# Kernel optimization log

Hardware: AMD Instinct MI355X
Metric: run time of the kernel (lower is better)

## Reference

```python
import jax, jax.numpy as jnp
import numpy as np

B, S, D = 128, 1024, 1024  # batch, seq_len, dim (ctx_dim == dim)


def setup_inputs() -> dict:
    key = jax.random.key(0)
    k1, k2, k3, k4, k5 = jax.random.split(key, 5)
    h = jax.random.normal(k1, (B, D), dtype=jnp.float32)
    context = jax.random.normal(k2, (B, S, D), dtype=jnp.float32)
    mask = jax.random.randint(k3, (B, S), 0, 2).astype(bool)
    # scale weights like nn.Linear default init (~U(-1/sqrt(fan_in), 1/sqrt(fan_in)))
    W_in = jax.random.normal(k4, (D, D), dtype=jnp.float32) / np.sqrt(D)
    W_out = jax.random.normal(k5, (D, 2 * D), dtype=jnp.float32) / np.sqrt(2 * D)
    return {"h": h, "context": context, "mask": mask, "W_in": W_in, "W_out": W_out}


def reference(h, context, mask, W_in, W_out):
    # target = linear_in(h): [B, ctx_dim]
    target = h @ W_in.T
    # attention scores: bmm(context, target) -> [B, S]
    attn = jnp.einsum('bsd,bd->bs', context, target)
    attn = jnp.where(mask, -jnp.inf, attn)
    attn = jax.nn.softmax(attn, axis=1)
    # weighted context: [B, D]
    weighted_context = jnp.einsum('bs,bsd->bd', attn, context)
    h_tilde = jnp.tanh(jnp.concatenate([weighted_context, h], axis=1) @ W_out.T)
    return (h_tilde, attn)
```

## Files before the change

kernel.cpp:

```cpp
#include <hip/hip_runtime.h>
#include <hip/hip_bf16.h>
#include <math.h>

#define BB 128
#define SS 1024
#define DD 1024
#define NC 8
#define SC (SS / NC)

#define OFF_TARGET 0
#define OFF_SCORES (BB * DD)
#define OFF_M      (OFF_SCORES + BB * SS)
#define OFF_L      (OFF_M + BB * NC)
#define OFF_WCP    (OFF_L + BB * NC)
#define OFF_WC     (OFF_WCP + BB * NC * DD)
#define OFF_FLAG   (OFF_WC + BB * DD)

__global__ void detect_mask(const unsigned char* __restrict__ mask,
                            int* __restrict__ flag)
{
    if (threadIdx.x == 0) {
        int isInt32 = 1;
        for (int i = 0; i < 256; ++i) {
            unsigned char b0 = mask[4 * i + 0];
            unsigned char b1 = mask[4 * i + 1];
            unsigned char b2 = mask[4 * i + 2];
            unsigned char b3 = mask[4 * i + 3];
            if (b1 | b2 | b3) { isInt32 = 0; break; }
            if (b0 > 1)       { isInt32 = 0; break; }
        }
        *flag = isInt32;
    }
}

__global__ __launch_bounds__(256) void gemm_nt(
    const float* __restrict__ A0, const float* __restrict__ A1,
    const float* __restrict__ Bm, float* __restrict__ Cout,
    int M, int N, int K, int applyTanh)
{
    __shared__ float As[16][64];
    __shared__ float Bs[32][65];

    const int tid  = threadIdx.x;
    const int bn0  = blockIdx.x * 32;
    const int bm0  = blockIdx.y * 16;
    const int r    = tid >> 5;
    const int ccol = tid & 31;

    const int ar = tid >> 4;
    const int ak = (tid & 15) << 2;

    float acc0 = 0.f, acc1 = 0.f;

    for (int k0 = 0; k0 < K; k0 += 64) {
        const float* Asrc = A0;
        int kk = k0;
        if (A1 != nullptr && k0 >= 1024) { Asrc = A1; kk = k0 - 1024; }
        float4 av = *(const float4*)(Asrc + (size_t)(bm0 + ar) * 1024 + kk + ak);
        *(float4*)&As[ar][ak] = av;

        #pragma unroll
        for (int u = 0; u < 2; ++u) {
            int idx4 = tid + u * 256;
            int c    = idx4 >> 4;
            int k    = (idx4 & 15) << 2;
            float4 bv = *(const float4*)(Bm + (size_t)(bn0 + c) * K + k0 + k);
            Bs[c][k + 0] = bv.x;
            Bs[c][k + 1] = bv.y;
            Bs[c][k + 2] = bv.z;
            Bs[c][k + 3] = bv.w;
        }
        __syncthreads();

        #pragma unroll
        for (int k = 0; k < 64; ++k) {
            float bv = Bs[ccol][k];
            acc0 = fmaf(As[r][k],     bv, acc0);
            acc1 = fmaf(As[r + 8][k], bv, acc1);
        }
        __syncthreads();
    }

    const int col = bn0 + ccol;
    float v0 = applyTanh ? tanhf(acc0) : acc0;
    float v1 = applyTanh ? tanhf(acc1) : acc1;
    Cout[(size_t)(bm0 + r) * N + col]     = v0;
    Cout[(size_t)(bm0 + r + 8) * N + col] = v1;
}

__global__ __launch_bounds__(256) void attn_pass(
    const float* __restrict__ ctx, const float* __restrict__ tgt,
    const unsigned char* __restrict__ mask_u8,
    const int* __restrict__ mask_flag,
    float* __restrict__ scores, float* __restrict__ m_part,
    float* __restrict__ l_part, float* __restrict__ wc_part)
{
    const int b    = blockIdx.y;
    const int ch   = blockIdx.x;
    const int tid  = threadIdx.x;
    const int w    = tid >> 6;
    const int lane = tid & 63;
    const int s0   = ch * SC;

    const int mflag = *mask_flag;
    const int* mask_i32 = (const int*)mask_u8;

    float4 t4[4];
    const float4* tp = (const float4*)(tgt + (size_t)b * DD);
    #pragma unroll
    for (int j = 0; j < 4; ++j) t4[j] = tp[j * 64 + lane];

    float m = -INFINITY, l = 0.f;
    float4 acc[4];
    #pragma unroll
    for (int j = 0; j < 4; ++j) acc[j] = make_float4(0.f, 0.f, 0.f, 0.f);

    float* srow = scores + (size_t)b * SS;

    for (int i = 0; i < SC / 4; ++i) {
        const int s = s0 + w + i * 4;
        const float4* row = (const float4*)(ctx + ((size_t)b * SS + s) * DD);
        float4 c4[4];
        #pragma unroll
        for (int j = 0; j < 4; ++j) c4[j] = row[j * 64 + lane];

        float part = 0.f;
        #pragma unroll
        for (int j = 0; j < 4; ++j) {
            part = fmaf(c4[j].x, t4[j].x, part);
            part = fmaf(c4[j].y, t4[j].y, part);
            part = fmaf(c4[j].z, t4[j].z, part);
            part = fmaf(c4[j].w, t4[j].w, part);
        }
        #pragma unroll
        for (int off = 32; off >= 1; off >>= 1)
            part += __shfl_xor(part, off, 64);

        const int mraw = mflag ? mask_i32[(size_t)b * SS + s]
                               : (int)mask_u8[(size_t)b * SS + s];
        const bool mk = (mraw != 0);
        const float sc = mk ? -INFINITY : part;
        if (lane == 0) srow[s] = sc;

        if (sc > m) {
            const float f = __expf(m - sc);
            l *= f;
            #pragma unroll
            for (int j = 0; j < 4; ++j) {
                acc[j].x *= f; acc[j].y *= f; acc[j].z *= f; acc[j].w *= f;
            }
            m = sc;
        }
        const float p = mk ? 0.f : __expf(sc - m);
        l += p;
        #pragma unroll
        for (int j = 0; j < 4; ++j) {
            acc[j].x = fmaf(p, c4[j].x, acc[j].x);
            acc[j].y = fmaf(p, c4[j].y, acc[j].y);
            acc[j].z = fmaf(p, c4[j].z, acc[j].z);
            acc[j].w = fmaf(p, c4[j].w, acc[j].w);
        }
    }

    __shared__ float sm[4], sl[4];
    __shared__ float sacc[4][DD];
    if (lane == 0) { sm[w] = m; sl[w] = l; }
    #pragma unroll
    for (int j = 0; j < 4; ++j)
        *(float4*)&sacc[w][j * 256 + lane * 4] = acc[j];
    __syncthreads();

    const float mb = fmaxf(fmaxf(sm[0], sm[1]), fmaxf(sm[2], sm[3]));
    const float f0 = __expf(sm[0] - mb);
    const float f1 = __expf(sm[1] - mb);
    const float f2 = __expf(sm[2] - mb);
    const float f3 = __expf(sm[3] - mb);
    const float lb = sl[0] * f0 + sl[1] * f1 + sl[2] * f2 + sl[3] * f3;

    const int d0 = tid * 4;
    float4 a0 = *(float4*)&sacc[0][d0];
    float4 a1 = *(float4*)&sacc[1][d0];
    float4 a2 = *(float4*)&sacc[2][d0];
    float4 a3 = *(float4*)&sacc[3][d0];
    float4 o;
    o.x = a0.x * f0 + a1.x * f1 + a2.x * f2 + a3.x * f3;
    o.y = a0.y * f0 + a1.y * f1 + a2.y * f2 + a3.y * f3;
    o.z = a0.z * f0 + a1.z * f1 + a2.z * f2 + a3.z * f3;
    o.w = a0.w * f0 + a1.w * f1 + a2.w * f2 + a3.w * f3;
    *(float4*)(wc_part + ((size_t)b * NC + ch) * DD + d0) = o;

    if (tid == 0) {
        m_part[b * NC + ch] = mb;
        l_part[b * NC + ch] = lb;
    }
}

__global__ __launch_bounds__(256) void combine(
    const float* __restrict__ m_part, const float* __restrict__ l_part,
    const float* __restrict__ wc_part, const float* __restrict__ scores,
    float* __restrict__ wc, float* __restrict__ attn_out)
{
    const int b = blockIdx.x;
    const int tid = threadIdx.x;

    float M = -INFINITY;
    #pragma unroll
    for (int c = 0; c < NC; ++c) M = fmaxf(M, m_part[b * NC + c]);
    float fc[NC];
    float L = 0.f;
    #pragma unroll
    for (int c = 0; c < NC; ++c) {
        fc[c] = __expf(m_part[b * NC + c] - M);
        L = fmaf(l_part[b * NC + c], fc[c], L);
    }
    const float invL = 1.f / L;

    const int d0 = tid * 4;
    float4 v = make_float4(0.f, 0.f, 0.f, 0.f);
    #pragma unroll
    for (int c = 0; c < NC; ++c) {
        float4 pv = *(const float4*)(wc_part + ((size_t)b * NC + c) * DD + d0);
        v.x = fmaf(pv.x, fc[c], v.x);
        v.y = fmaf(pv.y, fc[c], v.y);
        v.z = fmaf(pv.z, fc[c], v.z);
        v.w = fmaf(pv.w, fc[c], v.w);
    }
    v.x *= invL; v.y *= invL; v.z *= invL; v.w *= invL;
    *(float4*)(wc + (size_t)b * DD + d0) = v;

    for (int s = tid; s < SS; s += 256)
        attn_out[(size_t)b * SS + s] = __expf(scores[(size_t)b * SS + s] - M) * invL;
}

extern "C" void kernel_launch(void* const* d_in, const int* in_sizes, int n_in,
                              void* d_out, int out_size, void* d_ws, size_t ws_size,
                              hipStream_t stream)
{
    (void)in_sizes; (void)n_in; (void)out_size; (void)ws_size;

    const float* h     = (const float*)d_in[0];
    const float* ctx   = (const float*)d_in[1];
    const unsigned char* mask = (const unsigned char*)d_in[2];
    const float* W_in  = (const float*)d_in[3];
    const float* W_out = (const float*)d_in[4];

    float* out_h    = (float*)d_out;
    float* out_attn = out_h + (size_t)BB * DD;

    float* ws      = (float*)d_ws;
    float* target  = ws + OFF_TARGET;
    float* scores  = ws + OFF_SCORES;
    float* m_part  = ws + OFF_M;
    float* l_part  = ws + OFF_L;
    float* wc_part = ws + OFF_WCP;
    float* wc      = ws + OFF_WC;
    int*   mflag   = (int*)(ws + OFF_FLAG);

    detect_mask<<<1, 64, 0, stream>>>(mask, mflag);

    gemm_nt<<<dim3(32, 8), 256, 0, stream>>>(h, nullptr, W_in, target,
                                             BB, DD, 1024, 0);

    attn_pass<<<dim3(NC, BB), 256, 0, stream>>>(ctx, target, mask, mflag,
                                                scores, m_part, l_part, wc_part);

    combine<<<dim3(BB), 256, 0, stream>>>(m_part, l_part, wc_part, scores,
                                          wc, out_attn);

    gemm_nt<<<dim3(32, 8), 256, 0, stream>>>(wc, h, W_out, out_h,
                                             BB, DD, 2048, 1);
}
```

Before: 817.2 us.

## Use split-K register-tiled GEMMs and process four context rows per attention step

Replaces the small 16x32 GEMM with a 64x64 register-blocked tile (4x4 outputs per thread) split over K into eight partial buffers. A separate reduction kernel sums the partials and applies tanh. The attention pass now loads four contiguous rows per wave per step, so it batches the shuffle reductions, mask loads and online-softmax rescaling. The mask-detection loop is also parallelised across the wave. The cost is extra workspace traffic for the partials, two more kernel launches, and more registers per thread in the attention kernel.

```diff
diff --git a/kernel.cpp b/kernel.cpp
--- a/kernel.cpp
+++ b/kernel.cpp
@@ -7,85 +7,124 @@
 #define DD 1024
 #define NC 8
 #define SC (SS / NC)
-
-#define OFF_TARGET 0
-#define OFF_SCORES (BB * DD)
-#define OFF_M      (OFF_SCORES + BB * SS)
-#define OFF_L      (OFF_M + BB * NC)
-#define OFF_WCP    (OFF_L + BB * NC)
-#define OFF_WC     (OFF_WCP + BB * NC * DD)
-#define OFF_FLAG   (OFF_WC + BB * DD)
+#define KSPLIT 8
+
+#define OFF_TGT_PART 0
+#define OFF_TARGET   (OFF_TGT_PART + KSPLIT * BB * DD)
+#define OFF_SCORES   (OFF_TARGET + BB * DD)
+#define OFF_M        (OFF_SCORES + BB * SS)
+#define OFF_L        (OFF_M + BB * NC)
+#define OFF_WCP      (OFF_L + BB * NC)
+#define OFF_WC       (OFF_WCP + BB * NC * DD)
+#define OFF_OUT_PART (OFF_WC + BB * DD)
+#define OFF_FLAG     (OFF_OUT_PART + KSPLIT * BB * DD)
 
 __global__ void detect_mask(const unsigned char* __restrict__ mask,
                             int* __restrict__ flag)
 {
-    if (threadIdx.x == 0) {
-        int isInt32 = 1;
-        for (int i = 0; i < 256; ++i) {
-            unsigned char b0 = mask[4 * i + 0];
-            unsigned char b1 = mask[4 * i + 1];
-            unsigned char b2 = mask[4 * i + 2];
-            unsigned char b3 = mask[4 * i + 3];
-            if (b1 | b2 | b3) { isInt32 = 0; break; }
-            if (b0 > 1)       { isInt32 = 0; break; }
-        }
-        *flag = isInt32;
-    }
-}
-
-__global__ __launch_bounds__(256) void gemm_nt(
+    const int tid = threadIdx.x;
+    int ok = 1;
+    for (int i = tid; i < 256; i += 64) {
+        unsigned char b0 = mask[4 * i + 0];
+        unsigned char b1 = mask[4 * i + 1];
+        unsigned char b2 = mask[4 * i + 2];
+        unsigned char b3 = mask[4 * i + 3];
+        if ((b1 | b2 | b3) != 0 || b0 > 1) ok = 0;
+    }
+    int all_ok = __all(ok);
+    if (tid == 0) *flag = all_ok;
+}
+
+__global__ __launch_bounds__(256) void gemm_splitk(
     const float* __restrict__ A0, const float* __restrict__ A1,
-    const float* __restrict__ Bm, float* __restrict__ Cout,
-    int M, int N, int K, int applyTanh)
-{
-    __shared__ float As[16][64];
-    __shared__ float Bs[32][65];
-
-    const int tid  = threadIdx.x;
-    const int bn0  = blockIdx.x * 32;
-    const int bm0  = blockIdx.y * 16;
-    const int r    = tid >> 5;
-    const int ccol = tid & 31;
-
-    const int ar = tid >> 4;
-    const int ak = (tid & 15) << 2;
-
-    float acc0 = 0.f, acc1 = 0.f;
-
-    for (int k0 = 0; k0 < K; k0 += 64) {
+    const float* __restrict__ W, float* __restrict__ Cpart,
+    int N, int K)
+{
+    __shared__ float As_t[64][64];
+    __shared__ float Bs_t[64][64];
+
+    const int tid = threadIdx.x;
+    const int bn0 = blockIdx.x * 64;
+    const int bm0 = blockIdx.y * 64;
+    const int kchunk = K / KSPLIT;
+    const int kbase = blockIdx.z * kchunk;
+
+    const int lrow = tid >> 2;
+    const int lk   = (tid & 3) * 16;
+    const int tr4  = (tid >> 4) * 4;
+    const int tc4  = (tid & 15) * 4;
+
+    float4 acc[4];
+    #pragma unroll
+    for (int r = 0; r < 4; ++r) acc[r] = make_float4(0.f, 0.f, 0.f, 0.f);
+
+    for (int k0 = kbase; k0 < kbase + kchunk; k0 += 64) {
         const float* Asrc = A0;
         int kk = k0;
         if (A1 != nullptr && k0 >= 1024) { Asrc = A1; kk = k0 - 1024; }
-        float4 av = *(const float4*)(Asrc + (size_t)(bm0 + ar) * 1024 + kk + ak);
-        *(float4*)&As[ar][ak] = av;
-
-        #pragma unroll
-        for (int u = 0; u < 2; ++u) {
-            int idx4 = tid + u * 256;
-            int c    = idx4 >> 4;
-            int k    = (idx4 & 15) << 2;
-            float4 bv = *(const float4*)(Bm + (size_t)(bn0 + c) * K + k0 + k);
-            Bs[c][k + 0] = bv.x;
-            Bs[c][k + 1] = bv.y;
-            Bs[c][k + 2] = bv.z;
-            Bs[c][k + 3] = bv.w;
+
+        #pragma unroll
+        for (int j = 0; j < 4; ++j) {
+            float4 av = *(const float4*)(Asrc + (size_t)(bm0 + lrow) * 1024 + kk + lk + 4 * j);
+            As_t[lk + 4 * j + 0][lrow] = av.x;
+            As_t[lk + 4 * j + 1][lrow] = av.y;
+            As_t[lk + 4 * j + 2][lrow] = av.z;
+            As_t[lk + 4 * j + 3][lrow] = av.w;
+            float4 wv = *(const float4*)(W + (size_t)(bn0 + lrow) * K + k0 + lk + 4 * j);
+            Bs_t[lk + 4 * j + 0][lrow] = wv.x;
+            Bs_t[lk + 4 * j + 1][lrow] = wv.y;
+            Bs_t[lk + 4 * j + 2][lrow] = wv.z;
+            Bs_t[lk + 4 * j + 3][lrow] = wv.w;
         }
         __syncthreads();
 
         #pragma unroll
         for (int k = 0; k < 64; ++k) {
-            float bv = Bs[ccol][k];
-            acc0 = fmaf(As[r][k],     bv, acc0);
-            acc1 = fmaf(As[r + 8][k], bv, acc1);
+            float4 a = *(const float4*)&As_t[k][tr4];
+            float4 b = *(const float4*)&Bs_t[k][tc4];
+            acc[0].x = fmaf(a.x, b.x, acc[0].x);
+            acc[0].y = fmaf(a.x, b.y, acc[0].y);
+            acc[0].z = fmaf(a.x, b.z, acc[0].z);
+            acc[0].w = fmaf(a.x, b.w, acc[0].w);
+            acc[1].x = fmaf(a.y, b.x, acc[1].x);
+            acc[1].y = fmaf(a.y, b.y, acc[1].y);
+            acc[1].z = fmaf(a.y, b.z, acc[1].z);
+            acc[1].w = fmaf(a.y, b.w, acc[1].w);
+            acc[2].x = fmaf(a.z, b.x, acc[2].x);
+            acc[2].y = fmaf(a.z, b.y, acc[2].y);
+            acc[2].z = fmaf(a.z, b.z, acc[2].z);
+            acc[2].w = fmaf(a.z, b.w, acc[2].w);
+            acc[3].x = fmaf(a.w, b.x, acc[3].x);
+            acc[3].y = fmaf(a.w, b.y, acc[3].y);
+            acc[3].z = fmaf(a.w, b.z, acc[3].z);
+            acc[3].w = fmaf(a.w, b.w, acc[3].w);
         }
         __syncthreads();
     }
 
-    const int col = bn0 + ccol;
-    float v0 = applyTanh ? tanhf(acc0) : acc0;
-    float v1 = applyTanh ? tanhf(acc1) : acc1;
-    Cout[(size_t)(bm0 + r) * N + col]     = v0;
-    Cout[(size_t)(bm0 + r + 8) * N + col] = v1;
+    float* base = Cpart + ((size_t)blockIdx.z * BB + bm0 + tr4) * N + bn0 + tc4;
+    #pragma unroll
+    for (int r = 0; r < 4; ++r)
+        *(float4*)(base + (size_t)r * N) = acc[r];
+}
+
+__global__ __launch_bounds__(256) void reduce_part(
+    const float* __restrict__ part, float* __restrict__ out,
+    int n4, int applyTanh)
+{
+    const int i = blockIdx.x * 256 + threadIdx.x;
+    if (i >= n4) return;
+    const float4* p4 = (const float4*)part;
+    float4 s = p4[i];
+    #pragma unroll
+    for (int ks = 1; ks < KSPLIT; ++ks) {
+        float4 v = p4[(size_t)ks * n4 + i];
+        s.x += v.x; s.y += v.y; s.z += v.z; s.w += v.w;
+    }
+    if (applyTanh) {
+        s.x = tanhf(s.x); s.y = tanhf(s.y); s.z = tanhf(s.z); s.w = tanhf(s.w);
+    }
+    ((float4*)out)[i] = s;
 }
 
 __global__ __launch_bounds__(256) void attn_pass(
@@ -100,7 +139,7 @@
     const int tid  = threadIdx.x;
     const int w    = tid >> 6;
     const int lane = tid & 63;
-    const int s0   = ch * SC;
+    const int sbase = ch * SC + w * 32;
 
     const int mflag = *mask_flag;
     const int* mask_i32 = (const int*)mask_u8;
@@ -117,48 +156,80 @@
 
     float* srow = scores + (size_t)b * SS;
 
-    for (int i = 0; i < SC / 4; ++i) {
-        const int s = s0 + w + i * 4;
-        const float4* row = (const float4*)(ctx + ((size_t)b * SS + s) * DD);
-        float4 c4[4];
-        #pragma unroll
-        for (int j = 0; j < 4; ++j) c4[j] = row[j * 64 + lane];
-
-        float part = 0.f;
-        #pragma unroll
-        for (int j = 0; j < 4; ++j) {
-            part = fmaf(c4[j].x, t4[j].x, part);
-            part = fmaf(c4[j].y, t4[j].y, part);
-            part = fmaf(c4[j].z, t4[j].z, part);
-            part = fmaf(c4[j].w, t4[j].w, part);
-        }
-        #pragma unroll
-        for (int off = 32; off >= 1; off >>= 1)
-            part += __shfl_xor(part, off, 64);
-
-        const int mraw = mflag ? mask_i32[(size_t)b * SS + s]
-                               : (int)mask_u8[(size_t)b * SS + s];
-        const bool mk = (mraw != 0);
-        const float sc = mk ? -INFINITY : part;
-        if (lane == 0) srow[s] = sc;
-
-        if (sc > m) {
-            const float f = __expf(m - sc);
+    for (int g = 0; g < 8; ++g) {
+        const int s = sbase + g * 4;
+        const float4* r0 = (const float4*)(ctx + ((size_t)b * SS + s) * DD);
+
+        float4 c[4][4];
+        #pragma unroll
+        for (int rr = 0; rr < 4; ++rr)
+            #pragma unroll
+            for (int j = 0; j < 4; ++j)
+                c[rr][j] = r0[rr * 256 + j * 64 + lane];
+
+        float part[4];
+        #pragma unroll
+        for (int rr = 0; rr < 4; ++rr) {
+            float p = 0.f;
+            #pragma unroll
+            for (int j = 0; j < 4; ++j) {
+                p = fmaf(c[rr][j].x, t4[j].x, p);
+                p = fmaf(c[rr][j].y, t4[j].y, p);
+                p = fmaf(c[rr][j].z, t4[j].z, p);
+                p = fmaf(c[rr][j].w, t4[j].w, p);
+            }
+            part[rr] = p;
+        }
+        #pragma unroll
+        for (int off = 32; off >= 1; off >>= 1) {
+            #pragma unroll
+            for (int rr = 0; rr < 4; ++rr)
+                part[rr] += __shfl_xor(part[rr], off, 64);
+        }
+
+        int mk[4];
+        if (mflag) {
+            int4 mi = *(const int4*)(mask_i32 + (size_t)b * SS + s);
+            mk[0] = mi.x; mk[1] = mi.y; mk[2] = mi.z; mk[3] = mi.w;
+        } else {
+            uchar4 mu = *(const uchar4*)(mask_u8 + (size_t)b * SS + s);
+            mk[0] = mu.x; mk[1] = mu.y; mk[2] = mu.z; mk[3] = mu.w;
+        }
+        float sc[4];
+        #pragma unroll
+        for (int rr = 0; rr < 4; ++rr)
+            sc[rr] = mk[rr] ? -INFINITY : part[rr];
+
+        if (lane == 0)
+            *(float4*)(srow + s) = make_float4(sc[0], sc[1], sc[2], sc[3]);
+
+        const float gm = fmaxf(fmaxf(sc[0], sc[1]), fmaxf(sc[2], sc[3]));
+        if (gm > m) {
+            const float f = __expf(m - gm);
             l *= f;
             #pragma unroll
             for (int j = 0; j < 4; ++j) {
                 acc[j].x *= f; acc[j].y *= f; acc[j].z *= f; acc[j].w *= f;
             }
-            m = sc;
-        }
-        const float p = mk ? 0.f : __expf(sc - m);
-        l += p;
+            m = gm;
+        }
+        float p[4];
+        #pragma unroll
+        for (int rr = 0; rr < 4; ++rr)
+            p[rr] = mk[rr] ? 0.f : __expf(sc[rr] - m);
+        l += (p[0] + p[1]) + (p[2] + p[3]);
+
         #pragma unroll
         for (int j = 0; j < 4; ++j) {
-            acc[j].x = fmaf(p, c4[j].x, acc[j].x);
-            acc[j].y = fmaf(p, c4[j].y, acc[j].y);
-            acc[j].z = fmaf(p, c4[j].z, acc[j].z);
-            acc[j].w = fmaf(p, c4[j].w, acc[j].w);
+            float4 a = acc[j];
+            #pragma unroll
+            for (int rr = 0; rr < 4; ++rr) {
+                a.x = fmaf(p[rr], c[rr][j].x, a.x);
+                a.y = fmaf(p[rr], c[rr][j].y, a.y);
+                a.z = fmaf(p[rr], c[rr][j].z, a.z);
+                a.w = fmaf(p[rr], c[rr][j].w, a.w);
+            }
+            acc[j] = a;
         }
     }
 
@@ -247,19 +318,22 @@
     float* out_h    = (float*)d_out;
     float* out_attn = out_h + (size_t)BB * DD;
 
-    float* ws      = (float*)d_ws;
-    float* target  = ws + OFF_TARGET;
-    float* scores  = ws + OFF_SCORES;
-    float* m_part  = ws + OFF_M;
-    float* l_part  = ws + OFF_L;
-    float* wc_part = ws + OFF_WCP;
-    float* wc      = ws + OFF_WC;
-    int*   mflag   = (int*)(ws + OFF_FLAG);
+    float* ws       = (float*)d_ws;
+    float* tgt_part = ws + OFF_TGT_PART;
+    float* target   = ws + OFF_TARGET;
+    float* scores   = ws + OFF_SCORES;
+    float* m_part   = ws + OFF_M;
+    float* l_part   = ws + OFF_L;
+    float* wc_part  = ws + OFF_WCP;
+    float* wc       = ws + OFF_WC;
+    float* out_part = ws + OFF_OUT_PART;
+    int*   mflag    = (int*)(ws + OFF_FLAG);
 
     detect_mask<<<1, 64, 0, stream>>>(mask, mflag);
 
-    gemm_nt<<<dim3(32, 8), 256, 0, stream>>>(h, nullptr, W_in, target,
-                                             BB, DD, 1024, 0);
+    gemm_splitk<<<dim3(16, 2, KSPLIT), 256, 0, stream>>>(h, nullptr, W_in,
+                                                         tgt_part, DD, 1024);
+    reduce_part<<<dim3(128), 256, 0, stream>>>(tgt_part, target, BB * DD / 4, 0);
 
     attn_pass<<<dim3(NC, BB), 256, 0, stream>>>(ctx, target, mask, mflag,
                                                 scores, m_part, l_part, wc_part);
@@ -267,6 +341,7 @@
     combine<<<dim3(BB), 256, 0, stream>>>(m_part, l_part, wc_part, scores,
                                           wc, out_attn);
 
-    gemm_nt<<<dim3(32, 8), 256, 0, stream>>>(wc, h, W_out, out_h,
-                                             BB, DD, 2048, 1);
-}
+    gemm_splitk<<<dim3(16, 2, KSPLIT), 256, 0, stream>>>(wc, h, W_out,
+                                                         out_part, DD, 2048);
+    reduce_part<<<dim3(128), 256, 0, stream>>>(out_part, out_h, BB * DD / 4, 1);
+}
```

Measured after the change: 735.3 us. 1.11x faster.
